# Kernel tuning notes

Hardware: AMD Instinct MI355X
Metric: run time of the kernel (lower is better)

Reference implementation:

```python
import jax, jax.numpy as jnp
import numpy as np

N = 100000       # nodes
E = 1600000      # edges (avg degree 16)
F_IN = 128
F_HID = 64
F_OUT = 40
K = 10
ALPHA = 0.1


def setup_inputs() -> dict:
    key = jax.random.key(0)
    k1, k2, k3, k4, k5, k6 = jax.random.split(key, 6)
    x = jax.random.normal(k1, (N, F_IN), dtype=jnp.float32)
    edge_index = jax.random.randint(k2, (2, E), 0, N, dtype=jnp.int32)
    # Linear params (Kaiming-uniform-ish scale)
    W1 = jax.random.normal(k3, (F_IN, F_HID), dtype=jnp.float32) / np.sqrt(F_IN)
    b1 = jax.random.normal(k4, (F_HID,), dtype=jnp.float32) * 0.01
    W2 = jax.random.normal(k5, (F_HID, F_OUT), dtype=jnp.float32) / np.sqrt(F_HID)
    b2 = jax.random.normal(k6, (F_OUT,), dtype=jnp.float32) * 0.01
    return {"x": x, "edge_index": edge_index, "W1": W1, "b1": b1, "W2": W2, "b2": b2}


def _gcn_norm(edge_index, dtype):
    # add self loops, symmetric normalization D^{-1/2} (A+I) D^{-1/2}
    loops = jnp.arange(N, dtype=edge_index.dtype)
    src = jnp.concatenate([edge_index[0], loops])
    dst = jnp.concatenate([edge_index[1], loops])
    deg = jax.ops.segment_sum(jnp.ones_like(src, dtype=dtype), dst, num_segments=N)
    dinv = jnp.where(deg > 0, jax.lax.rsqrt(deg), 0.0).astype(dtype)
    norm = dinv[src] * dinv[dst]  # [E + N]
    return src, dst, norm


def _appnp(x, src, dst, norm):
    h = x  # teleport target
    def step(xc, _):
        agg = jax.ops.segment_sum(xc[src] * norm[:, None], dst, num_segments=N)
        return (1.0 - ALPHA) * agg + ALPHA * h, None
    out, _ = jax.lax.scan(step, x, None, length=K)
    return out


def reference(x, edge_index, W1, b1, W2, b2):
    src, dst, norm = _gcn_norm(edge_index, x.dtype)
    # layer 1: Linear -> relu -> (dropout p=0) -> APPNP
    h = jax.nn.relu(x @ W1 + b1)
    h = _appnp(h, src, dst, norm)
    # layer 2: Linear -> relu -> APPNP
    h = jax.nn.relu(h @ W2 + b2)
    h = _appnp(h, src, dst, norm)
    return jax.nn.log_softmax(h, axis=1)
```

## Files before the change

kernel.cpp:

```cpp
#include <hip/hip_runtime.h>
#include <hip/hip_fp16.h>
#include <hip/hip_fp8.h>

namespace {
constexpr int NN = 100000;
constexpr int NE = 1600000;
constexpr int FIN = 128, FHID = 64, FOUT = 40;
constexpr float ALPHA = 0.1f;
constexpr int SLOTS = 64;
constexpr int SB = 40;
constexpr int ECHUNK = 200000;

typedef int v4i __attribute__((ext_vector_type(4)));
typedef unsigned int v2u __attribute__((ext_vector_type(2)));
typedef unsigned int v4u __attribute__((ext_vector_type(4)));
typedef float v2f __attribute__((ext_vector_type(2)));
typedef float v4f __attribute__((ext_vector_type(4)));

#if __has_builtin(__builtin_amdgcn_cvt_pk_f32_fp8) && __has_builtin(__builtin_amdgcn_cvt_pk_fp8_f32)
#define HW_FP8 1
#else
#define HW_FP8 0
#endif

__device__ __forceinline__ ushort f2h(float v) {
  union { __half h; ushort u; } cv;
  cv.h = __float2half_rn(v);
  return cv.u;
}

__device__ __forceinline__ void acc8_fp8(v2u w, float* a) {
#if HW_FP8
  v2f p0 = __builtin_amdgcn_cvt_pk_f32_fp8((int)w.x, false);
  v2f p1 = __builtin_amdgcn_cvt_pk_f32_fp8((int)w.x, true);
  v2f p2 = __builtin_amdgcn_cvt_pk_f32_fp8((int)w.y, false);
  v2f p3 = __builtin_amdgcn_cvt_pk_f32_fp8((int)w.y, true);
  a[0] += p0.x; a[1] += p0.y; a[2] += p1.x; a[3] += p1.y;
  a[4] += p2.x; a[5] += p2.y; a[6] += p3.x; a[7] += p3.y;
#else
  union { v2u w; unsigned char b[8]; } cv;
  cv.w = w;
#pragma unroll
  for (int k = 0; k < 8; k++) {
    __hip_fp8_e4m3 h;
    h.__x = cv.b[k];
    a[k] += (float)h;
  }
#endif
}

__device__ __forceinline__ v2u enc8_fp8(const float* o) {
#if HW_FP8
  int d0 = __builtin_amdgcn_cvt_pk_fp8_f32(o[0], o[1], 0, false);
  d0 = __builtin_amdgcn_cvt_pk_fp8_f32(o[2], o[3], d0, true);
  int d1 = __builtin_amdgcn_cvt_pk_fp8_f32(o[4], o[5], 0, false);
  d1 = __builtin_amdgcn_cvt_pk_fp8_f32(o[6], o[7], d1, true);
  v2u r;
  r.x = (unsigned int)d0;
  r.y = (unsigned int)d1;
  return r;
#else
  union { v2u w; unsigned char b[8]; } cv;
#pragma unroll
  for (int k = 0; k < 8; k++) {
    __hip_fp8_e4m3 h(o[k]);
    cv.b[k] = h.__x;
  }
  return cv.w;
#endif
}

__device__ __forceinline__ unsigned char enc1_fp8(float v) {
#if HW_FP8
  return (unsigned char)(__builtin_amdgcn_cvt_pk_fp8_f32(v, v, 0, false) & 0xff);
#else
  __hip_fp8_e4m3 h(v);
  return h.__x;
#endif
}

__global__ void k_zero(int* cnt) {
  int i = blockIdx.x * 256 + threadIdx.x;
  if (i < NN) cnt[i] = 0;
}

__global__ void k_fill_ell(const int* __restrict__ src, const int* __restrict__ dst,
                           int* __restrict__ cnt, int* __restrict__ ell, int ebase) {
  int e = ebase + blockIdx.x * 256 + threadIdx.x;
  if (e >= ebase + ECHUNK || e >= NE) return;
  int s = src[e], d = dst[e];
  int p = atomicAdd(&cnt[d], 1);
  if (p < SLOTS) ell[(d << 6) + p] = s;
}

__global__ void k_dinv(const int* __restrict__ cnt, float2* __restrict__ dd) {
  int i = blockIdx.x * 256 + threadIdx.x;
  if (i < NN) {
    float di = rsqrtf((float)(cnt[i] + 1));
    dd[i] = make_float2(di, 0.9f * di * di);
  }
}

__global__ __launch_bounds__(256) void k_mlp(const float* __restrict__ x,
                                             const float* __restrict__ W1,
                                             const float* __restrict__ b1,
                                             const float* __restrict__ W2,
                                             const float2* __restrict__ dd,
                                             float* __restrict__ h2x,
                                             ushort* __restrict__ u0,
                                             unsigned char* __restrict__ uq) {
  __shared__ float w1s[FIN * FHID];
  __shared__ float w2s[FHID * FOUT];
  __shared__ float hs[16][FHID];
  for (int i = threadIdx.x; i < FIN * FHID / 4; i += 256)
    ((float4*)w1s)[i] = ((const float4*)W1)[i];
  for (int i = threadIdx.x; i < FHID * FOUT / 4; i += 256)
    ((float4*)w2s)[i] = ((const float4*)W2)[i];
  __syncthreads();
  int ln = threadIdx.x >> 4;
  int ch = threadIdx.x & 15;
  int node = blockIdx.x * 16 + ln;
  const float* xr = x + (size_t)node * FIN;
  float4 acc = {0, 0, 0, 0};
  for (int k = 0; k < FIN; k += 4) {
    float4 xv = *(const float4*)(xr + k);
    float4 w0 = ((const float4*)(w1s + (k + 0) * FHID))[ch];
    float4 w1 = ((const float4*)(w1s + (k + 1) * FHID))[ch];
    float4 w2 = ((const float4*)(w1s + (k + 2) * FHID))[ch];
    float4 w3 = ((const float4*)(w1s + (k + 3) * FHID))[ch];
    acc.x += xv.x * w0.x + xv.y * w1.x + xv.z * w2.x + xv.w * w3.x;
    acc.y += xv.x * w0.y + xv.y * w1.y + xv.z * w2.y + xv.w * w3.y;
    acc.z += xv.x * w0.z + xv.y * w1.z + xv.z * w2.z + xv.w * w3.z;
    acc.w += xv.x * w0.w + xv.y * w1.w + xv.z * w2.w + xv.w * w3.w;
  }
  float4 bb = ((const float4*)b1)[ch];
  hs[ln][ch * 4 + 0] = fmaxf(acc.x + bb.x, 0.f);
  hs[ln][ch * 4 + 1] = fmaxf(acc.y + bb.y, 0.f);
  hs[ln][ch * 4 + 2] = fmaxf(acc.z + bb.z, 0.f);
  hs[ln][ch * 4 + 3] = fmaxf(acc.w + bb.w, 0.f);
  __syncthreads();
  for (int o = threadIdx.x; o < 16 * FOUT; o += 256) {
    int nd = o / FOUT;
    int c = o - nd * FOUT;
    float a = 0.f;
#pragma unroll
    for (int k = 0; k < FHID; k++) a += hs[nd][k] * w2s[k * FOUT + c];
    int gn = blockIdx.x * 16 + nd;
    float u = dd[gn].x * a;
    h2x[(size_t)gn * FOUT + c] = a;
    u0[(size_t)gn * FOUT + c] = f2h(u);
    uq[(size_t)gn * SB + c] = enc1_fp8(u);
  }
}

__device__ __forceinline__ void gather_ell(const int* __restrict__ ell,
                                           const unsigned char* __restrict__ u,
                                           int node, int ch, int deg, float* a) {
#pragma unroll
  for (int k = 0; k < 8; k++) a[k] = 0.f;
  const unsigned char* ub = u + ch * 8;
  const v4i* ip = (const v4i*)ell + ((size_t)node << 4);
  v2u ws = *(const v2u*)(ub + (size_t)node * SB);
  v4i q0 = ip[0];
  v4i q1 = ip[1];
  acc8_fp8(ws, a);
  int j = 0;
  for (; j + 8 <= deg; j += 8) {
    int g = (j >> 2) + 2;
    v4i n0 = ip[g > 15 ? 15 : g];
    v4i n1 = ip[g + 1 > 15 ? 15 : g + 1];
    v2u w0 = *(const v2u*)(ub + (size_t)q0.x * SB);
    v2u w1 = *(const v2u*)(ub + (size_t)q0.y * SB);
    v2u w2 = *(const v2u*)(ub + (size_t)q0.z * SB);
    v2u w3 = *(const v2u*)(ub + (size_t)q0.w * SB);
    v2u w4 = *(const v2u*)(ub + (size_t)q1.x * SB);
    v2u w5 = *(const v2u*)(ub + (size_t)q1.y * SB);
    v2u w6 = *(const v2u*)(ub + (size_t)q1.z * SB);
    v2u w7 = *(const v2u*)(ub + (size_t)q1.w * SB);
    acc8_fp8(w0, a);
    acc8_fp8(w1, a);
    acc8_fp8(w2, a);
    acc8_fp8(w3, a);
    acc8_fp8(w4, a);
    acc8_fp8(w5, a);
    acc8_fp8(w6, a);
    acc8_fp8(w7, a);
    q0 = n0;
    q1 = n1;
  }
  if (j + 4 <= deg) {
    v2u w0 = *(const v2u*)(ub + (size_t)q0.x * SB);
    v2u w1 = *(const v2u*)(ub + (size_t)q0.y * SB);
    v2u w2 = *(const v2u*)(ub + (size_t)q0.z * SB);
    v2u w3 = *(const v2u*)(ub + (size_t)q0.w * SB);
    acc8_fp8(w0, a);
    acc8_fp8(w1, a);
    acc8_fp8(w2, a);
    acc8_fp8(w3, a);
    q0 = q1;
    j += 4;
  }
  if (j < deg) {
    int rr = deg - j;
    acc8_fp8(*(const v2u*)(ub + (size_t)q0.x * SB), a);
    if (rr > 1) acc8_fp8(*(const v2u*)(ub + (size_t)q0.y * SB), a);
    if (rr > 2) acc8_fp8(*(const v2u*)(ub + (size_t)q0.z * SB), a);
  }
}

#define APPNP_HDR(cntp)                            \
  int tid = threadIdx.x;                           \
  int nd = tid / 5, ch = tid - nd * 5;             \
  int node = blockIdx.x * 64 + nd;                 \
  if (node >= NN) return;                          \
  int deg = (cntp)[node];                          \
  deg = deg > SLOTS ? SLOTS : deg;

__device__ __forceinline__ void store_h8(ushort* p, const float* v) {
  union { v4u u; __half h[8]; } cv;
#pragma unroll
  for (int k = 0; k < 8; k++) cv.h[k] = __float2half_rn(v[k]);
  *(v4u*)p = cv.u;
}

__global__ __launch_bounds__(320, 6) void k_mid(const int* __restrict__ cnt,
                                                const int* __restrict__ ell,
                                                const float2* __restrict__ dd,
                                                const ushort* __restrict__ u0,
                                                const unsigned char* __restrict__ u,
                                                unsigned char* __restrict__ un) {
  APPNP_HDR(cnt)
  union { v4u q; __half h[8]; } t0;
  t0.q = *(const v4u*)(u0 + (size_t)node * FOUT + ch * 8);
  float c9 = dd[node].y;
  float a[8];
  gather_ell(ell, u, node, ch, deg, a);
  float o[8];
#pragma unroll
  for (int k = 0; k < 8; k++) o[k] = c9 * a[k] + ALPHA * __half2float(t0.h[k]);
  v2u st = enc8_fp8(o);
  *(v2u*)(un + (size_t)node * SB + ch * 8) = st;
}

__global__ __launch_bounds__(320, 6) void k_final1(const int* __restrict__ cnt,
                                                   const int* __restrict__ ell,
                                                   const float2* __restrict__ dd,
                                                   const float* __restrict__ b2,
                                                   const float* __restrict__ h2x,
                                                   const unsigned char* __restrict__ u,
                                                   ushort* __restrict__ gh,
                                                   ushort* __restrict__ u0n,
                                                   unsigned char* __restrict__ uqn) {
  APPNP_HDR(cnt)
  float di = dd[node].x;
  v4f h0 = __builtin_nontemporal_load((const v4f*)(h2x + (size_t)node * FOUT + ch * 8));
  v4f h1 = __builtin_nontemporal_load((const v4f*)(h2x + (size_t)node * FOUT + ch * 8 + 4));
  const float* bb = b2 + ch * 8;
  float a[8];
  gather_ell(ell, u, node, ch, deg, a);
  float t9 = 0.9f * di;
  float hx[8] = {h0.x, h0.y, h0.z, h0.w, h1.x, h1.y, h1.z, h1.w};
  float g[8], ug[8];
#pragma unroll
  for (int k = 0; k < 8; k++) {
    float z = t9 * a[k] + ALPHA * hx[k] + bb[k];
    g[k] = fmaxf(z, 0.f);
    ug[k] = di * g[k];
  }
  store_h8(gh + (size_t)node * FOUT + ch * 8, g);
  store_h8(u0n + (size_t)node * FOUT + ch * 8, ug);
  v2u st = enc8_fp8(ug);
  *(v2u*)(uqn + (size_t)node * SB + ch * 8) = st;
}

__global__ __launch_bounds__(320, 6) void k_final2(const int* __restrict__ cnt,
                                                   const int* __restrict__ ell,
                                                   const float2* __restrict__ dd,
                                                   const ushort* __restrict__ gh,
                                                   const unsigned char* __restrict__ u,
                                                   ushort* __restrict__ zh) {
  APPNP_HDR(cnt)
  union { v4u q; __half h[8]; } hv;
  hv.q = *(const v4u*)(gh + (size_t)node * FOUT + ch * 8);
  float t9 = 0.9f * dd[node].x;
  float a[8];
  gather_ell(ell, u, node, ch, deg, a);
  float o[8];
#pragma unroll
  for (int k = 0; k < 8; k++) o[k] = t9 * a[k] + ALPHA * __half2float(hv.h[k]);
  store_h8(zh + (size_t)node * FOUT + ch * 8, o);
}

__global__ void k_logsoftmax(const ushort* __restrict__ in, float* __restrict__ out) {
  int i = blockIdx.x * 256 + threadIdx.x;
  if (i >= NN) return;
  union { v4u q; __half h[8]; } v[5];
  const v4u* r = (const v4u*)(in + (size_t)i * FOUT);
  float f[40];
  float m = -1e30f;
#pragma unroll
  for (int j = 0; j < 5; j++) {
    v[j].q = r[j];
#pragma unroll
    for (int k = 0; k < 8; k++) {
      f[j * 8 + k] = __half2float(v[j].h[k]);
      m = fmaxf(m, f[j * 8 + k]);
    }
  }
  float sum = 0.f;
#pragma unroll
  for (int j = 0; j < 40; j++) sum += expf(f[j] - m);
  float lse = m + logf(sum);
  float4* o = (float4*)(out + (size_t)i * FOUT);
#pragma unroll
  for (int j = 0; j < 10; j++) {
    float4 w = {f[j * 4] - lse, f[j * 4 + 1] - lse, f[j * 4 + 2] - lse, f[j * 4 + 3] - lse};
    o[j] = w;
  }
}

}

extern "C" void kernel_launch(void* const* d_in, const int* in_sizes, int n_in,
                              void* d_out, int out_size, void* d_ws, size_t ws_size,
                              hipStream_t stream) {
  const float* x = (const float*)d_in[0];
  const int* ei = (const int*)d_in[1];
  const int* src = ei;
  const int* dst = ei + NE;
  const float* W1 = (const float*)d_in[2];
  const float* b1 = (const float*)d_in[3];
  const float* W2 = (const float*)d_in[4];
  const float* b2 = (const float*)d_in[5];
  float* out = (float*)d_out;

  char* ws = (char*)d_ws;
  size_t off = 0;
  auto alloc = [&](size_t bytes) -> void* {
    void* p = ws + off;
    off += (bytes + 255) & ~(size_t)255;
    return p;
  };
  int* cnt          = (int*)alloc((size_t)NN * 4);
  float2* dd        = (float2*)alloc((size_t)NN * 8);
  int* ell          = (int*)alloc((size_t)NN * SLOTS * 4);
  float* h2x        = (float*)alloc((size_t)NN * FOUT * 4);
  ushort* u0h       = (ushort*)alloc((size_t)NN * FOUT * 2);
  ushort* gh        = (ushort*)alloc((size_t)NN * FOUT * 2);
  ushort* zh        = (ushort*)alloc((size_t)NN * FOUT * 2);
  unsigned char* q0 = (unsigned char*)alloc((size_t)NN * SB);
  unsigned char* qA = (unsigned char*)alloc((size_t)NN * SB);
  unsigned char* qB = (unsigned char*)alloc((size_t)NN * SB);

  k_zero<<<(NN + 255) / 256, 256, 0, stream>>>(cnt);
  for (int c = 0; c < NE / ECHUNK; c++)
    k_fill_ell<<<(ECHUNK + 255) / 256, 256, 0, stream>>>(src, dst, cnt, ell, c * ECHUNK);
  k_dinv<<<(NN + 255) / 256, 256, 0, stream>>>(cnt, dd);

  k_mlp<<<NN / 16, 256, 0, stream>>>(x, W1, b1, W2, dd, h2x, u0h, q0);

  int agrid = (NN + 63) / 64;
  const unsigned char* cu = q0;
  for (int it = 0; it < 9; it++) {
    unsigned char* nx = (it & 1) ? qB : qA;
    k_mid<<<agrid, 320, 0, stream>>>(cnt, ell, dd, u0h, cu, nx);
    cu = nx;
  }
  k_final1<<<agrid, 320, 0, stream>>>(cnt, ell, dd, b2, h2x, cu, gh, u0h, q0);

  cu = q0;
  for (int it = 0; it < 9; it++) {
    unsigned char* nx = (it & 1) ? qB : qA;
    k_mid<<<agrid, 320, 0, stream>>>(cnt, ell, dd, u0h, cu, nx);
    cu = nx;
  }
  k_final2<<<agrid, 320, 0, stream>>>(cnt, ell, dd, gh, cu, zh);

  k_logsoftmax<<<(NN + 255) / 256, 256, 0, stream>>>(zh, out);
}
```

Measured before the change: 706.3 us.

## Rewrite MLP kernel with fp16 MFMA and vectorized fp8 stores

The two-layer linear part now runs on 16x16x32 fp16 MFMA instructions instead of scalar FP32 FMAs. Weights are transposed into padded fp16 shared memory, and each wave handles 16 nodes per block of 64. Outputs are written as float4, packed halfs and packed 4-byte fp8 words instead of single scalars. This cuts ALU work and improves store coalescing, but rounds x, the weights and the hidden activations to fp16, which lowers precision.

```diff
diff --git a/kernel.cpp b/kernel.cpp
--- a/kernel.cpp
+++ b/kernel.cpp
@@ -16,6 +16,7 @@
 typedef unsigned int v4u __attribute__((ext_vector_type(4)));
 typedef float v2f __attribute__((ext_vector_type(2)));
 typedef float v4f __attribute__((ext_vector_type(4)));
+typedef _Float16 half8 __attribute__((ext_vector_type(8)));
 
 #if __has_builtin(__builtin_amdgcn_cvt_pk_f32_fp8) && __has_builtin(__builtin_amdgcn_cvt_pk_fp8_f32)
 #define HW_FP8 1
@@ -70,12 +71,16 @@
 #endif
 }
 
-__device__ __forceinline__ unsigned char enc1_fp8(float v) {
+__device__ __forceinline__ unsigned int enc4_fp8(float a, float b, float c, float d) {
 #if HW_FP8
-  return (unsigned char)(__builtin_amdgcn_cvt_pk_fp8_f32(v, v, 0, false) & 0xff);
+  int d0 = __builtin_amdgcn_cvt_pk_fp8_f32(a, b, 0, false);
+  d0 = __builtin_amdgcn_cvt_pk_fp8_f32(c, d, d0, true);
+  return (unsigned int)d0;
 #else
-  __hip_fp8_e4m3 h(v);
-  return h.__x;
+  union { unsigned char b4[4]; unsigned int u; } cv;
+  __hip_fp8_e4m3 h0(a), h1(b), h2(c), h3(d);
+  cv.b4[0] = h0.__x; cv.b4[1] = h1.__x; cv.b4[2] = h2.__x; cv.b4[3] = h3.__x;
+  return cv.u;
 #endif
 }
 
@@ -101,55 +106,98 @@
   }
 }
 
-__global__ __launch_bounds__(256) void k_mlp(const float* __restrict__ x,
-                                             const float* __restrict__ W1,
-                                             const float* __restrict__ b1,
-                                             const float* __restrict__ W2,
-                                             const float2* __restrict__ dd,
-                                             float* __restrict__ h2x,
-                                             ushort* __restrict__ u0,
-                                             unsigned char* __restrict__ uq) {
-  __shared__ float w1s[FIN * FHID];
-  __shared__ float w2s[FHID * FOUT];
-  __shared__ float hs[16][FHID];
-  for (int i = threadIdx.x; i < FIN * FHID / 4; i += 256)
-    ((float4*)w1s)[i] = ((const float4*)W1)[i];
-  for (int i = threadIdx.x; i < FHID * FOUT / 4; i += 256)
-    ((float4*)w2s)[i] = ((const float4*)W2)[i];
+__global__ __launch_bounds__(256, 3) void k_mlp(const float* __restrict__ x,
+                                                const float* __restrict__ W1,
+                                                const float* __restrict__ b1,
+                                                const float* __restrict__ W2,
+                                                const float2* __restrict__ dd,
+                                                float* __restrict__ h2x,
+                                                ushort* __restrict__ u0,
+                                                unsigned char* __restrict__ uq) {
+  __shared__ _Float16 w1t[64 * 136];
+  __shared__ _Float16 w2t[48 * 72];
+  __shared__ unsigned int ht[4 * 16 * 36];
+
+  int tid = threadIdx.x;
+  for (int i = tid; i < 2048; i += 256) {
+    float4 v = ((const float4*)W1)[i];
+    int k = i >> 4;
+    int c0 = (i & 15) * 4;
+    w1t[(c0 + 0) * 136 + k] = (_Float16)v.x;
+    w1t[(c0 + 1) * 136 + k] = (_Float16)v.y;
+    w1t[(c0 + 2) * 136 + k] = (_Float16)v.z;
+    w1t[(c0 + 3) * 136 + k] = (_Float16)v.w;
+  }
+  for (int i = tid; i < 2560; i += 256) {
+    int k = i / 40, c = i - k * 40;
+    w2t[c * 72 + k] = (_Float16)W2[i];
+  }
+  for (int i = tid; i < 576; i += 256) w2t[2880 + i] = (_Float16)0.f;
   __syncthreads();
-  int ln = threadIdx.x >> 4;
-  int ch = threadIdx.x & 15;
-  int node = blockIdx.x * 16 + ln;
-  const float* xr = x + (size_t)node * FIN;
-  float4 acc = {0, 0, 0, 0};
-  for (int k = 0; k < FIN; k += 4) {
-    float4 xv = *(const float4*)(xr + k);
-    float4 w0 = ((const float4*)(w1s + (k + 0) * FHID))[ch];
-    float4 w1 = ((const float4*)(w1s + (k + 1) * FHID))[ch];
-    float4 w2 = ((const float4*)(w1s + (k + 2) * FHID))[ch];
-    float4 w3 = ((const float4*)(w1s + (k + 3) * FHID))[ch];
-    acc.x += xv.x * w0.x + xv.y * w1.x + xv.z * w2.x + xv.w * w3.x;
-    acc.y += xv.x * w0.y + xv.y * w1.y + xv.z * w2.y + xv.w * w3.y;
-    acc.z += xv.x * w0.z + xv.y * w1.z + xv.z * w2.z + xv.w * w3.z;
-    acc.w += xv.x * w0.w + xv.y * w1.w + xv.z * w2.w + xv.w * w3.w;
-  }
-  float4 bb = ((const float4*)b1)[ch];
-  hs[ln][ch * 4 + 0] = fmaxf(acc.x + bb.x, 0.f);
-  hs[ln][ch * 4 + 1] = fmaxf(acc.y + bb.y, 0.f);
-  hs[ln][ch * 4 + 2] = fmaxf(acc.z + bb.z, 0.f);
-  hs[ln][ch * 4 + 3] = fmaxf(acc.w + bb.w, 0.f);
-  __syncthreads();
-  for (int o = threadIdx.x; o < 16 * FOUT; o += 256) {
-    int nd = o / FOUT;
-    int c = o - nd * FOUT;
-    float a = 0.f;
-#pragma unroll
-    for (int k = 0; k < FHID; k++) a += hs[nd][k] * w2s[k * FOUT + c];
-    int gn = blockIdx.x * 16 + nd;
-    float u = dd[gn].x * a;
-    h2x[(size_t)gn * FOUT + c] = a;
-    u0[(size_t)gn * FOUT + c] = f2h(u);
-    uq[(size_t)gn * SB + c] = enc1_fp8(u);
+
+  int wid = tid >> 6, lane = tid & 63;
+  int g = lane >> 4, n = lane & 15;
+  int node = blockIdx.x * 64 + wid * 16 + n;
+  int nodeL = node < NN ? node : NN - 1;
+  const float* xr = x + (size_t)nodeL * FIN;
+
+  v4f acc1[4] = {};
+#pragma unroll
+  for (int kk = 0; kk < 4; kk++) {
+    const float4* xp = (const float4*)(xr + kk * 32 + g * 8);
+    float4 xa = xp[0], xb = xp[1];
+    half8 bx;
+    bx[0] = (_Float16)xa.x; bx[1] = (_Float16)xa.y;
+    bx[2] = (_Float16)xa.z; bx[3] = (_Float16)xa.w;
+    bx[4] = (_Float16)xb.x; bx[5] = (_Float16)xb.y;
+    bx[6] = (_Float16)xb.z; bx[7] = (_Float16)xb.w;
+#pragma unroll
+    for (int mt = 0; mt < 4; mt++) {
+      half8 af = *(const half8*)(w1t + (mt * 16 + n) * 136 + kk * 32 + g * 8);
+      acc1[mt] = __builtin_amdgcn_mfma_f32_16x16x32_f16(af, bx, acc1[mt], 0, 0, 0);
+    }
+  }
+
+  unsigned int* hw = ht + wid * 576 + n * 36;
+#pragma unroll
+  for (int mt = 0; mt < 4; mt++) {
+    float4 bb = *(const float4*)(b1 + mt * 16 + g * 4);
+    union { _Float16 h[4]; uint2 u; } pk;
+    pk.h[0] = (_Float16)fmaxf(acc1[mt][0] + bb.x, 0.f);
+    pk.h[1] = (_Float16)fmaxf(acc1[mt][1] + bb.y, 0.f);
+    pk.h[2] = (_Float16)fmaxf(acc1[mt][2] + bb.z, 0.f);
+    pk.h[3] = (_Float16)fmaxf(acc1[mt][3] + bb.w, 0.f);
+    *(uint2*)(hw + mt * 8 + g * 2) = pk.u;
+  }
+
+  v4f acc2[3] = {};
+#pragma unroll
+  for (int kk = 0; kk < 2; kk++) {
+    half8 bh = *(const half8*)((const _Float16*)(hw + kk * 16 + g * 4));
+#pragma unroll
+    for (int mt2 = 0; mt2 < 3; mt2++) {
+      half8 af = *(const half8*)(w2t + (mt2 * 16 + n) * 72 + kk * 32 + g * 8);
+      acc2[mt2] = __builtin_amdgcn_mfma_f32_16x16x32_f16(af, bh, acc2[mt2], 0, 0, 0);
+    }
+  }
+
+  if (node < NN) {
+    float di = dd[node].x;
+#pragma unroll
+    for (int mt2 = 0; mt2 < 3; mt2++) {
+      int c0 = mt2 * 16 + g * 4;
+      if (c0 < FOUT) {
+        float y0 = acc2[mt2][0], y1 = acc2[mt2][1];
+        float y2 = acc2[mt2][2], y3 = acc2[mt2][3];
+        *(float4*)(h2x + (size_t)node * FOUT + c0) = make_float4(y0, y1, y2, y3);
+        float u0v = di * y0, u1v = di * y1, u2v = di * y2, u3v = di * y3;
+        union { ushort s[4]; uint2 q; } hq;
+        hq.s[0] = f2h(u0v); hq.s[1] = f2h(u1v);
+        hq.s[2] = f2h(u2v); hq.s[3] = f2h(u3v);
+        *(uint2*)(u0 + (size_t)node * FOUT + c0) = hq.q;
+        *(unsigned int*)(uq + (size_t)node * SB + c0) = enc4_fp8(u0v, u1v, u2v, u3v);
+      }
+    }
   }
 }
 
@@ -357,7 +405,7 @@
     k_fill_ell<<<(ECHUNK + 255) / 256, 256, 0, stream>>>(src, dst, cnt, ell, c * ECHUNK);
   k_dinv<<<(NN + 255) / 256, 256, 0, stream>>>(cnt, dd);
 
-  k_mlp<<<NN / 16, 256, 0, stream>>>(x, W1, b1, W2, dd, h2x, u0h, q0);
+  k_mlp<<<(NN + 63) / 64, 256, 0, stream>>>(x, W1, b1, W2, dd, h2x, u0h, q0);
 
   int agrid = (NN + 63) / 64;
   const unsigned char* cu = q0;
```

Measured after the change: 653.6 us. 1.08x faster.
